# Kernel optimization log

Hardware: AMD Instinct MI355X
Metric: run time of the kernel (lower is better)

## Reference

```python
import jax, jax.numpy as jnp
import numpy as np

N = 100000   # nodes
E = 500000   # edges per relation
R = 3        # relations (etypes)
L = 2        # layers
F = 300      # input features
H = 256      # hidden
C = 23       # classes


def setup_inputs() -> dict:
    key = jax.random.key(0)
    ks = jax.random.split(key, 12)
    s = 0.05
    return {
        "x": jax.random.normal(ks[0], (N, F), jnp.float32),
        "edge_src": jax.random.randint(ks[1], (R, E), 0, N, dtype=jnp.int32),
        "edge_dst": jax.random.randint(ks[2], (R, E), 0, N, dtype=jnp.int32),
        "W_feat": jax.random.normal(ks[3], (F, H), jnp.float32) * s,
        "b_feat": jnp.zeros((H,), jnp.float32),
        "g_feat": jnp.ones((H,), jnp.float32),
        "beta_feat": jnp.zeros((H,), jnp.float32),
        "gcn_W": jax.random.normal(ks[4], (L, R, H, H), jnp.float32) * s,
        "gcn_b": jnp.zeros((L, R, H), jnp.float32),
        "skip_W": jax.random.normal(ks[5], (L, H, H), jnp.float32) * s,
        "skip_b": jnp.zeros((L, H), jnp.float32),
        "bn_g": jnp.ones((L, H), jnp.float32),
        "bn_b": jnp.zeros((L, H), jnp.float32),
        "W_c1": jax.random.normal(ks[6], (H, H), jnp.float32) * s,
        "b_c1": jnp.zeros((H,), jnp.float32),
        "g_c": jnp.ones((H,), jnp.float32),
        "beta_c": jnp.zeros((H,), jnp.float32),
        "W_c2": jax.random.normal(ks[7], (H, C), jnp.float32) * s,
        "b_c2": jnp.zeros((C,), jnp.float32),
    }


def _bn(h, g, b):
    # BatchNorm1d, training-mode batch stats (biased var), eps=1e-5
    m = h.mean(0)
    v = jnp.mean((h - m) ** 2, 0)
    return g * (h - m) * jax.lax.rsqrt(v + 1e-5) + b


def _het_forward(x, edge_src, edge_dst, W_feat, b_feat, g_feat, beta_feat,
                 gcn_W, gcn_b, skip_W, skip_b, bn_g, bn_b,
                 W_c1, b_c1, g_c, beta_c, W_c2, b_c2):
    seg = jax.ops.segment_sum
    ones = jnp.ones((E,), jnp.float32)
    # feat_reduce: Linear + BN + ReLU
    h = jax.nn.relu(_bn(x @ W_feat + b_feat, g_feat, beta_feat))  # [N, H]
    for l in range(L):
        h_res = h @ skip_W[l] + skip_b[l]
        rel = []
        for r in range(R):  # per-relation GraphConv (DGL norm='both')
            src, dst = edge_src[r], edge_dst[r]
            dout = jnp.clip(seg(ones, src, num_segments=N), 1.0, None)
            din = jnp.clip(seg(ones, dst, num_segments=N), 1.0, None)
            xs = h * jax.lax.rsqrt(dout)[:, None]          # src-normalize
            m = seg(xs[src], dst, num_segments=N)          # gather-scatter
            m = m * jax.lax.rsqrt(din)[:, None]            # dst-normalize
            rel.append(m @ gcn_W[l, r] + gcn_b[l, r])
        h = jnp.mean(jnp.stack(rel, 0), 0)  # het_combine='mean'
        h = h + h_res
        h = jax.nn.leaky_relu(_bn(h, bn_g[l], bn_b[l]), 0.01)
        # dropout is identity in eval mode
    # classification head
    h = jax.nn.relu(_bn(h @ W_c1 + b_c1, g_c, beta_c))
    return h @ W_c2 + b_c2  # [N, C]


def reference(x, edge_src, edge_dst, W_feat, b_feat, g_feat, beta_feat,
              gcn_W, gcn_b, skip_W, skip_b, bn_g, bn_b,
              W_c1, b_c1, g_c, beta_c, W_c2, b_c2):
    return _het_forward(x, edge_src, edge_dst, W_feat, b_feat, g_feat,
                        beta_feat, gcn_W, gcn_b, skip_W, skip_b, bn_g, bn_b,
                        W_c1, b_c1, g_c, beta_c, W_c2, b_c2)
```

## Files before the change

kernel.cpp:

```cpp
#include <hip/hip_runtime.h>

#define NN 100000
#define EE 500000
#define RR 3
#define LL 2
#define FF 300
#define HH 256
#define CC 23
#define MPAD 100096
#define SCHUNK 2048
#define SNB ((NN + SCHUNK - 1) / SCHUNK)

static inline int cdiv_h(int a, int b) { return (a + b - 1) / b; }

typedef __attribute__((ext_vector_type(8))) short bf16x8;
typedef __attribute__((ext_vector_type(4))) float f32x4;
typedef __attribute__((ext_vector_type(4))) unsigned short u16x4;

__device__ inline unsigned short f2bf(float f) {
    union { float f; unsigned int u; } v; v.f = f;
    unsigned int r = v.u + 0x7fff + ((v.u >> 16) & 1);
    return (unsigned short)(r >> 16);
}
__device__ inline float bf2f(unsigned short u) {
    union { unsigned int u; float f; } v; v.u = ((unsigned int)u) << 16;
    return v.f;
}
__device__ inline void gl_lds16(const void* g, void* l) {
    __builtin_amdgcn_global_load_lds((const __attribute__((address_space(1))) unsigned int*)g,
                                     (__attribute__((address_space(3))) unsigned int*)l,
                                     16, 0, 0);
}

__global__ void hist_kernel(const int* __restrict__ src, const int* __restrict__ dst,
                            int* __restrict__ cnt_out, int* __restrict__ cnt_in,
                            int RE, int Eper) {
    int i = blockIdx.x * blockDim.x + threadIdx.x;
    if (i >= RE) return;
    int r = i / Eper;
    atomicAdd(&cnt_out[r * NN + src[i]], 1);
    atomicAdd(&cnt_in[r * NN + dst[i]], 1);
}

__global__ void rs_kernel(const int* __restrict__ cnt_out, const int* __restrict__ cnt_in,
                          float* __restrict__ rs_out, float* __restrict__ rs_in, int total) {
    int i = blockIdx.x * blockDim.x + threadIdx.x;
    if (i >= total) return;
    rs_out[i] = rsqrtf(fmaxf((float)cnt_out[i], 1.0f));
    rs_in[i]  = rsqrtf(fmaxf((float)cnt_in[i], 1.0f));
}

__global__ __launch_bounds__(256) void scan_a(const int* __restrict__ cnt, int* __restrict__ bsum) {
    int r = blockIdx.y, b = blockIdx.x, t = threadIdx.x;
    const int* c = cnt + (size_t)r * NN;
    int base = b * SCHUNK;
    int s = 0;
    for (int i = t; i < SCHUNK; i += 256) {
        int idx = base + i;
        if (idx < NN) s += c[idx];
    }
#pragma unroll
    for (int o = 1; o < 64; o <<= 1) s += __shfl_xor(s, o);
    __shared__ int sh[4];
    if ((t & 63) == 0) sh[t >> 6] = s;
    __syncthreads();
    if (t == 0) bsum[r * SNB + b] = sh[0] + sh[1] + sh[2] + sh[3];
}

__global__ void scan_b(int* __restrict__ bsum, int* __restrict__ offs) {
    int r = threadIdx.x;
    if (r >= RR) return;
    int* bs = bsum + r * SNB;
    int run = 0;
    for (int i = 0; i < SNB; i++) { int v = bs[i]; bs[i] = run; run += v; }
    offs[(size_t)r * (NN + 1) + NN] = run;
}

__global__ __launch_bounds__(256) void scan_c(const int* __restrict__ cnt, const int* __restrict__ bsum,
                                              int* __restrict__ offs, int* __restrict__ cur) {
    int r = blockIdx.y, b = blockIdx.x, t = threadIdx.x;
    const int* c = cnt + (size_t)r * NN;
    int base = b * SCHUNK + t * 8;
    int v[8]; int s = 0;
#pragma unroll
    for (int j = 0; j < 8; j++) {
        int idx = base + j;
        v[j] = (idx < NN) ? c[idx] : 0;
        s += v[j];
    }
    __shared__ int sh[256];
    sh[t] = s;
    __syncthreads();
    for (int d = 1; d < 256; d <<= 1) {
        int x = (t >= d) ? sh[t - d] : 0;
        __syncthreads();
        sh[t] += x;
        __syncthreads();
    }
    int run = sh[t] - s + bsum[r * SNB + b];
    int* orow = offs + (size_t)r * (NN + 1);
    int* crow = cur + (size_t)r * NN;
#pragma unroll
    for (int j = 0; j < 8; j++) {
        int idx = base + j;
        if (idx < NN) { orow[idx] = run; crow[idx] = run; }
        run += v[j];
    }
}

__global__ void fill_kernel(const int* __restrict__ src, const int* __restrict__ dst,
                            const float* __restrict__ rs_out,
                            int* __restrict__ cur, int2* __restrict__ srcw,
                            int RE, int Eper) {
    int i = blockIdx.x * blockDim.x + threadIdx.x;
    if (i >= RE) return;
    int r = i / Eper;
    int d = dst[i];
    int s = src[i];
    float w = rs_out[r * NN + s];
    int pos = atomicAdd(&cur[r * NN + d], 1);
    srcw[(size_t)r * Eper + pos] = make_int2(s, __float_as_int(w));
}

__global__ __launch_bounds__(256) void convert_x(const float* __restrict__ x, unsigned short* __restrict__ xpad) {
    int idx = blockIdx.x * blockDim.x + threadIdx.x;
    if (idx >= MPAD * 80) return;
    int row = idx / 80, c4 = (idx - row * 80) * 4;
    ushort4 o;
    if (row < NN && c4 + 3 < FF) {
        float4 v = *(const float4*)(x + (size_t)row * FF + c4);
        o.x = f2bf(v.x); o.y = f2bf(v.y); o.z = f2bf(v.z); o.w = f2bf(v.w);
    } else {
        o.x = 0; o.y = 0; o.z = 0; o.w = 0;
    }
    *(ushort4*)(xpad + (size_t)row * 320 + c4) = o;
}

__global__ void wprep_feat(const float* __restrict__ W, unsigned short* __restrict__ Bt) {
    int n = blockIdx.x;
    int k = threadIdx.x;
    float v = (k < FF) ? W[(size_t)k * HH + n] : 0.f;
    Bt[(size_t)n * 320 + k] = f2bf(v);
}

__global__ void wprep_layer(const float* __restrict__ skipW, const float* __restrict__ gcnW,
                            unsigned short* __restrict__ Bt) {
    int idx = blockIdx.x * blockDim.x + threadIdx.x;
    int n = idx >> 10, k = idx & 1023;
    int seg = k >> 8, k2 = k & 255;
    float v = (seg == 0) ? skipW[(size_t)k2 * HH + n]
                         : gcnW[(size_t)(seg - 1) * HH * HH + (size_t)k2 * HH + n] * (1.0f / 3.0f);
    Bt[(size_t)n * 1024 + k] = f2bf(v);
}

__global__ void bias_layer(const float* __restrict__ skip_b, const float* __restrict__ gcn_b,
                           float* __restrict__ bias) {
    int t = threadIdx.x;
    bias[t] = skip_b[t] + (gcn_b[t] + gcn_b[HH + t] + gcn_b[2 * HH + t]) * (1.0f / 3.0f);
}

__global__ void wprep_c1(const float* __restrict__ W, unsigned short* __restrict__ Bt) {
    int idx = blockIdx.x * blockDim.x + threadIdx.x;
    int n = idx >> 8, k = idx & 255;
    Bt[(size_t)n * HH + k] = f2bf(W[(size_t)k * HH + n]);
}

__global__ void wprep_c2(const float* __restrict__ W, unsigned short* __restrict__ Bt) {
    int n = blockIdx.x;
    int k = threadIdx.x;
    float v = (n < CC) ? W[(size_t)k * CC + n] : 0.f;
    Bt[(size_t)n * HH + k] = f2bf(v);
}

__global__ __launch_bounds__(256) void agg_bf16(unsigned short* __restrict__ hcat,
                                                const int* __restrict__ offs_all,
                                                const int2* __restrict__ srcw_all,
                                                const float* __restrict__ rs_in_all) {
    int r = blockIdx.y;
    const int* offs = offs_all + (size_t)r * (NN + 1);
    const int2* srcw = srcw_all + (size_t)r * EE;
    const float* rs_i = rs_in_all + (size_t)r * NN;
    int wave = threadIdx.x >> 6;
    int lane = threadIdx.x & 63;
    int node = blockIdx.x * 4 + wave;
    if (node >= NN) return;
    int s0 = __builtin_amdgcn_readfirstlane(offs[node]);
    int s1 = __builtin_amdgcn_readfirstlane(offs[node + 1]);
    int cnt = s1 - s0;
    const int2* ew = srcw + s0;
    const unsigned short* hb = hcat + lane * 4;
    float a0 = 0.f, a1 = 0.f, a2 = 0.f, a3 = 0.f;
    int k = 0;
    for (; k + 8 <= cnt; k += 8) {
        int2 e[8];
#pragma unroll
        for (int q = 0; q < 8; q++) e[q] = ew[k + q];
        ushort4 hv[8];
#pragma unroll
        for (int q = 0; q < 8; q++) hv[q] = *(const ushort4*)(hb + (size_t)e[q].x * 1024);
#pragma unroll
        for (int q = 0; q < 8; q++) {
            float u = __int_as_float(e[q].y);
            a0 += u * bf2f(hv[q].x); a1 += u * bf2f(hv[q].y);
            a2 += u * bf2f(hv[q].z); a3 += u * bf2f(hv[q].w);
        }
    }
    if (k + 4 <= cnt) {
        int2 e[4];
#pragma unroll
        for (int q = 0; q < 4; q++) e[q] = ew[k + q];
        ushort4 hv[4];
#pragma unroll
        for (int q = 0; q < 4; q++) hv[q] = *(const ushort4*)(hb + (size_t)e[q].x * 1024);
#pragma unroll
        for (int q = 0; q < 4; q++) {
            float u = __int_as_float(e[q].y);
            a0 += u * bf2f(hv[q].x); a1 += u * bf2f(hv[q].y);
            a2 += u * bf2f(hv[q].z); a3 += u * bf2f(hv[q].w);
        }
        k += 4;
    }
    int rem = cnt - k;
    if (rem > 0) {
        int2 e[3];
#pragma unroll
        for (int q = 0; q < 3; q++) {
            int kk = k + q; if (kk > cnt - 1) kk = cnt - 1;
            e[q] = ew[kk];
        }
        ushort4 hv[3];
#pragma unroll
        for (int q = 0; q < 3; q++) hv[q] = *(const ushort4*)(hb + (size_t)e[q].x * 1024);
        float u0 = __int_as_float(e[0].y);
        float u1 = rem > 1 ? __int_as_float(e[1].y) : 0.f;
        float u2 = rem > 2 ? __int_as_float(e[2].y) : 0.f;
        a0 += u0 * bf2f(hv[0].x) + u1 * bf2f(hv[1].x) + u2 * bf2f(hv[2].x);
        a1 += u0 * bf2f(hv[0].y) + u1 * bf2f(hv[1].y) + u2 * bf2f(hv[2].y);
        a2 += u0 * bf2f(hv[0].z) + u1 * bf2f(hv[1].z) + u2 * bf2f(hv[2].z);
        a3 += u0 * bf2f(hv[0].w) + u1 * bf2f(hv[1].w) + u2 * bf2f(hv[2].w);
    }
    float wi = rs_i[node];
    u16x4 o;
    o.x = f2bf(a0 * wi); o.y = f2bf(a1 * wi);
    o.z = f2bf(a2 * wi); o.w = f2bf(a3 * wi);
    __builtin_nontemporal_store(o, (u16x4*)(hcat + (size_t)node * 1024 + 256 * (r + 1) + lane * 4));
}

__global__ __launch_bounds__(512, 2) void mfma_gemm(const unsigned short* __restrict__ A, int ldA,
                                                    const unsigned short* __restrict__ Bt,
                                                    const float* __restrict__ bias,
                                                    void* __restrict__ Cv, int ldC,
                                                    int Nstore, int K, int c_bf16,
                                                    float* __restrict__ stats) {
    __shared__ unsigned short lds[2][24576];
    int tid = threadIdx.x;
    int w = tid >> 6, lane = tid & 63;
    int quad = lane >> 4, lr = lane & 15;
    int bm = blockIdx.y * 128;
    int wm = w >> 2, wn = w & 3;
    int lrow = lane >> 2;
    int lslot = lane & 3;

    f32x4 acc[4][4];
#pragma unroll
    for (int i = 0; i < 4; i++)
#pragma unroll
        for (int j = 0; j < 4; j++) acc[i][j] = (f32x4){0.f, 0.f, 0.f, 0.f};

    const int NT = K >> 6;

    auto stage = [&](int bi, int t) {
        int k0 = t << 6;
        int rA = w * 16 + lrow;
        int cgA = lslot ^ ((rA >> 1) & 3);
#pragma unroll
        for (int h = 0; h < 2; h++) {
            gl_lds16(A + (size_t)(bm + rA) * ldA + k0 + h * 32 + cgA * 8,
                     &lds[bi][h * 4096 + w * 512]);
#pragma unroll
            for (int c = 0; c < 2; c++) {
                int cc = w * 2 + c;
                int rB = cc * 16 + lrow;
                int cgB = lslot ^ ((rB >> 1) & 3);
                gl_lds16(Bt + (size_t)rB * K + k0 + h * 32 + cgB * 8,
                         &lds[bi][8192 + h * 8192 + cc * 512]);
            }
        }
    };

    stage(0, 0);
    asm volatile("s_waitcnt vmcnt(0)" ::: "memory");
    __builtin_amdgcn_s_barrier();
    asm volatile("" ::: "memory");

    int cur = 0;
    for (int t = 0; t < NT; t++) {
        if (t + 1 < NT) stage(cur ^ 1, t + 1);
#pragma unroll
        for (int h = 0; h < 2; h++) {
            bf16x8 af[4], bfr[4];
#pragma unroll
            for (int i = 0; i < 4; i++) {
                int r = wm * 64 + i * 16 + lr;
                int s = quad ^ ((r >> 1) & 3);
                af[i] = *(const bf16x8*)&lds[cur][h * 4096 + r * 32 + s * 8];
            }
#pragma unroll
            for (int j = 0; j < 4; j++) {
                int n = wn * 64 + j * 16 + lr;
                int s = quad ^ ((n >> 1) & 3);
                bfr[j] = *(const bf16x8*)&lds[cur][8192 + h * 8192 + n * 32 + s * 8];
            }
#pragma unroll
            for (int i = 0; i < 4; i++)
#pragma unroll
                for (int j = 0; j < 4; j++)
                    acc[i][j] = __builtin_amdgcn_mfma_f32_16x16x32_bf16(af[i], bfr[j], acc[i][j], 0, 0, 0);
        }
        if (t + 1 < NT) {
            asm volatile("s_waitcnt vmcnt(0)" ::: "memory");
            __builtin_amdgcn_s_barrier();
            asm volatile("" ::: "memory");
        }
        cur ^= 1;
    }

    __syncthreads();

    if (c_bf16) {
        unsigned short* ldsC = &lds[0][0];
#pragma unroll
        for (int j = 0; j < 4; j++) {
            int col = wn * 64 + j * 16 + lr;
            float bv = bias ? bias[col] : 0.f;
            float ssum = 0.f, ssq = 0.f;
#pragma unroll
            for (int i = 0; i < 4; i++) {
#pragma unroll
                for (int v = 0; v < 4; v++) {
                    int row = wm * 64 + i * 16 + quad * 4 + v;
                    float val = acc[i][j][v] + bv;
                    ldsC[row * 264 + col] = f2bf(val);
                    if (bm + row < NN) { ssum += val; ssq += val * val; }
                }
            }
            if (stats) {
                ssum += __shfl_xor(ssum, 16); ssum += __shfl_xor(ssum, 32);
                ssq  += __shfl_xor(ssq, 16);  ssq  += __shfl_xor(ssq, 32);
                if (quad == 0) {
                    atomicAdd(&stats[col], ssum);
                    atomicAdd(&stats[HH + col], ssq);
                }
            }
        }
        __syncthreads();
        int row = tid >> 2, seg = tid & 3;
        if (bm + row < NN) {
            const unsigned short* srcp = ldsC + row * 264 + seg * 64;
            unsigned short* dstp = (unsigned short*)Cv + (size_t)(bm + row) * ldC + seg * 64;
#pragma unroll
            for (int q = 0; q < 8; q++)
                *(uint4*)(dstp + q * 8) = *(const uint4*)(srcp + q * 8);
        }
    } else {
        float* Cf = (float*)Cv;
#pragma unroll
        for (int j = 0; j < 4; j++) {
            int col = wn * 64 + j * 16 + lr;
            if (col >= Nstore) continue;
            float bv = bias ? bias[col] : 0.f;
#pragma unroll
            for (int i = 0; i < 4; i++) {
#pragma unroll
                for (int v = 0; v < 4; v++) {
                    int row = bm + wm * 64 + i * 16 + quad * 4 + v;
                    if (row < NN) Cf[(size_t)row * ldC + col] = acc[i][j][v] + bv;
                }
            }
        }
    }
}

__global__ void bn_coef(const float* __restrict__ stats, const float* __restrict__ g,
                        const float* __restrict__ b, float* __restrict__ coef, float invM) {
    int c = threadIdx.x;
    float mean = stats[c] * invM;
    float var = stats[HH + c] * invM - mean * mean;
    float inv = rsqrtf(var + 1e-5f);
    float sc = g[c] * inv;
    coef[c] = sc;
    coef[HH + c] = b[c] - mean * sc;
}

__global__ __launch_bounds__(256) void bn_apply_v(const unsigned short* __restrict__ Z,
                                                  const float* __restrict__ coef,
                                                  unsigned short* __restrict__ out, int act) {
    int idx = blockIdx.x * blockDim.x + threadIdx.x;
    if (idx >= NN * 32) return;
    int row = idx >> 5, cg = (idx & 31) * 8;
    union { uint4 u; unsigned short s[8]; } zin, zo;
    zin.u = *(const uint4*)(Z + (size_t)row * HH + cg);
    f32x4 sc0 = *(const f32x4*)(coef + cg);
    f32x4 sc1 = *(const f32x4*)(coef + cg + 4);
    f32x4 sh0 = *(const f32x4*)(coef + HH + cg);
    f32x4 sh1 = *(const f32x4*)(coef + HH + cg + 4);
#pragma unroll
    for (int j = 0; j < 8; j++) {
        float sc = (j < 4) ? sc0[j] : sc1[j - 4];
        float sh = (j < 4) ? sh0[j] : sh1[j - 4];
        float v = bf2f(zin.s[j]) * sc + sh;
        if (act == 1) v = fmaxf(v, 0.f);
        else v = (v < 0.f) ? 0.01f * v : v;
        zo.s[j] = f2bf(v);
    }
    *(uint4*)(out + (size_t)row * 1024 + cg) = zo.u;
}

extern "C" void kernel_launch(void* const* d_in, const int* in_sizes, int n_in,
                              void* d_out, int out_size, void* d_ws, size_t ws_size,
                              hipStream_t stream) {
    const float* x        = (const float*)d_in[0];
    const int*   esrc     = (const int*)d_in[1];
    const int*   edst     = (const int*)d_in[2];
    const float* W_feat   = (const float*)d_in[3];
    const float* b_feat   = (const float*)d_in[4];
    const float* g_feat   = (const float*)d_in[5];
    const float* beta_feat= (const float*)d_in[6];
    const float* gcn_W    = (const float*)d_in[7];
    const float* gcn_b    = (const float*)d_in[8];
    const float* skip_W   = (const float*)d_in[9];
    const float* skip_b   = (const float*)d_in[10];
    const float* bn_g     = (const float*)d_in[11];
    const float* bn_b     = (const float*)d_in[12];
    const float* W_c1     = (const float*)d_in[13];
    const float* b_c1     = (const float*)d_in[14];
    const float* g_c      = (const float*)d_in[15];
    const float* beta_c   = (const float*)d_in[16];
    const float* W_c2     = (const float*)d_in[17];
    const float* b_c2     = (const float*)d_in[18];
    float* out = (float*)d_out;
    (void)in_sizes; (void)n_in; (void)out_size; (void)ws_size;

    char* w = (char*)d_ws;
    size_t off = 0;
    auto alloc = [&](size_t bytes) { void* p = w + off; off += (bytes + 255) & ~(size_t)255; return p; };
    unsigned short* hcat = (unsigned short*)alloc((size_t)MPAD * 1024 * 2);
    unsigned short* xpad = hcat;
    unsigned short* c_acc = (unsigned short*)alloc((size_t)NN * HH * 2);
    float* f_stats = (float*)alloc(4 * 2 * HH * 4);
    float* f_coef  = (float*)alloc(2 * HH * 4);
    float* f_rs_out = (float*)alloc((size_t)RR * NN * 4);
    float* f_rs_in  = (float*)alloc((size_t)RR * NN * 4);
    int* i_cnt_out = (int*)alloc((size_t)RR * NN * 4);
    int* i_cnt_in  = (int*)alloc((size_t)RR * NN * 4);
    int* i_off     = (int*)alloc((size_t)RR * (NN + 1) * 4);
    int* i_cur     = (int*)alloc((size_t)RR * NN * 4);
    int2* i_srcw   = (int2*)alloc((size_t)RR * EE * 8);
    int* i_bsum    = (int*)alloc((size_t)RR * SNB * 4);
    unsigned short* Bt_feat = (unsigned short*)alloc(256 * 320 * 2);
    unsigned short* Bt_l0   = (unsigned short*)alloc(256 * 1024 * 2);
    unsigned short* Bt_l1   = (unsigned short*)alloc(256 * 1024 * 2);
    unsigned short* Bt_c1   = (unsigned short*)alloc(256 * 256 * 2);
    unsigned short* Bt_c2   = (unsigned short*)alloc(256 * 256 * 2);
    float* bias_l0 = (float*)alloc(HH * 4);
    float* bias_l1 = (float*)alloc(HH * 4);

    const float invM = 1.0f / (float)NN;
    const int RE = RR * EE;

    (void)hipMemsetAsync(i_cnt_out, 0, (size_t)RR * NN * 4, stream);
    (void)hipMemsetAsync(i_cnt_in, 0, (size_t)RR * NN * 4, stream);
    (void)hipMemsetAsync(f_stats, 0, 4 * 2 * HH * 4, stream);
    hist_kernel<<<cdiv_h(RE, 256), 256, 0, stream>>>(esrc, edst, i_cnt_out, i_cnt_in, RE, EE);
    rs_kernel<<<cdiv_h(RR * NN, 256), 256, 0, stream>>>(i_cnt_out, i_cnt_in, f_rs_out, f_rs_in, RR * NN);
    scan_a<<<dim3(SNB, RR), 256, 0, stream>>>(i_cnt_in, i_bsum);
    scan_b<<<1, 64, 0, stream>>>(i_bsum, i_off);
    scan_c<<<dim3(SNB, RR), 256, 0, stream>>>(i_cnt_in, i_bsum, i_off, i_cur);
    fill_kernel<<<cdiv_h(RE, 256), 256, 0, stream>>>(esrc, edst, f_rs_out, i_cur, i_srcw, RE, EE);

    convert_x<<<cdiv_h(MPAD * 80, 256), 256, 0, stream>>>(x, xpad);
    wprep_feat<<<256, 320, 0, stream>>>(W_feat, Bt_feat);
    wprep_layer<<<1024, 256, 0, stream>>>(skip_W, gcn_W, Bt_l0);
    wprep_layer<<<1024, 256, 0, stream>>>(skip_W + (size_t)HH * HH, gcn_W + (size_t)RR * HH * HH, Bt_l1);
    bias_layer<<<1, 256, 0, stream>>>(skip_b, gcn_b, bias_l0);
    bias_layer<<<1, 256, 0, stream>>>(skip_b + HH, gcn_b + (size_t)RR * HH, bias_l1);
    wprep_c1<<<256, 256, 0, stream>>>(W_c1, Bt_c1);
    wprep_c2<<<256, 256, 0, stream>>>(W_c2, Bt_c2);

    dim3 grid_G(1, MPAD / 128);
    const int nblk_a = cdiv_h(NN * 32, 256);
    float* st0 = f_stats;
    float* st1 = f_stats + 2 * HH;
    float* st2 = f_stats + 4 * HH;
    float* st3 = f_stats + 6 * HH;

    mfma_gemm<<<grid_G, 512, 0, stream>>>(xpad, 320, Bt_feat, b_feat, c_acc, HH, HH, 320, 1, st0);
    bn_coef<<<1, 256, 0, stream>>>(st0, g_feat, beta_feat, f_coef, invM);
    bn_apply_v<<<nblk_a, 256, 0, stream>>>(c_acc, f_coef, hcat, 1);

    for (int l = 0; l < LL; l++) {
        agg_bf16<<<dim3(cdiv_h(NN, 4), RR), 256, 0, stream>>>(hcat, i_off, i_srcw, f_rs_in);
        float* st = l ? st2 : st1;
        mfma_gemm<<<grid_G, 512, 0, stream>>>(hcat, 1024, l ? Bt_l1 : Bt_l0,
                                              l ? bias_l1 : bias_l0, c_acc, HH, HH, 1024, 1, st);
        bn_coef<<<1, 256, 0, stream>>>(st, bn_g + (size_t)l * HH, bn_b + (size_t)l * HH, f_coef, invM);
        bn_apply_v<<<nblk_a, 256, 0, stream>>>(c_acc, f_coef, hcat, 2);
    }

    mfma_gemm<<<grid_G, 512, 0, stream>>>(hcat, 1024, Bt_c1, b_c1, c_acc, HH, HH, 256, 1, st3);
    bn_coef<<<1, 256, 0, stream>>>(st3, g_c, beta_c, f_coef, invM);
    bn_apply_v<<<nblk_a, 256, 0, stream>>>(c_acc, f_coef, hcat + 256, 1);
    mfma_gemm<<<grid_G, 512, 0, stream>>>(hcat + 256, 1024, Bt_c2, b_c2, out, CC, CC, 256, 0, nullptr);
}
```

Baseline: 1.212 ms.

## Load GEMM B fragments directly from global memory and shrink LDS for occupancy

The B (weight) operand is no longer staged through LDS. Each wave now reads its B fragments straight from global memory into registers every K-step, and only A stays double-buffered in LDS. LDS shrinks to a single array sized for the epilogue, and launch bounds are raised to 4 blocks per CU to allow more concurrent blocks. The trade is more redundant global and L2 traffic for B across waves and blocks, plus higher register pressure under the tighter bound, possibly with spills. The B loads are also issued synchronously before the MFMA loop, so their latency may not be hidden.

```diff
diff --git a/kernel.cpp b/kernel.cpp
--- a/kernel.cpp
+++ b/kernel.cpp
@@ -246,13 +246,13 @@
     __builtin_nontemporal_store(o, (u16x4*)(hcat + (size_t)node * 1024 + 256 * (r + 1) + lane * 4));
 }
 
-__global__ __launch_bounds__(512, 2) void mfma_gemm(const unsigned short* __restrict__ A, int ldA,
+__global__ __launch_bounds__(512, 4) void mfma_gemm(const unsigned short* __restrict__ A, int ldA,
                                                     const unsigned short* __restrict__ Bt,
                                                     const float* __restrict__ bias,
                                                     void* __restrict__ Cv, int ldC,
                                                     int Nstore, int K, int c_bf16,
                                                     float* __restrict__ stats) {
-    __shared__ unsigned short lds[2][24576];
+    __shared__ unsigned short lds[33792];
     int tid = threadIdx.x;
     int w = tid >> 6, lane = tid & 63;
     int quad = lane >> 4, lr = lane & 15;
@@ -269,53 +269,48 @@
 
     const int NT = K >> 6;
 
-    auto stage = [&](int bi, int t) {
+    const unsigned short* Bbase = Bt + (size_t)(wn * 64 + lr) * K + quad * 8;
+
+    auto stageA = [&](int bi, int t) {
         int k0 = t << 6;
         int rA = w * 16 + lrow;
         int cgA = lslot ^ ((rA >> 1) & 3);
 #pragma unroll
         for (int h = 0; h < 2; h++) {
             gl_lds16(A + (size_t)(bm + rA) * ldA + k0 + h * 32 + cgA * 8,
-                     &lds[bi][h * 4096 + w * 512]);
-#pragma unroll
-            for (int c = 0; c < 2; c++) {
-                int cc = w * 2 + c;
-                int rB = cc * 16 + lrow;
-                int cgB = lslot ^ ((rB >> 1) & 3);
-                gl_lds16(Bt + (size_t)rB * K + k0 + h * 32 + cgB * 8,
-                         &lds[bi][8192 + h * 8192 + cc * 512]);
-            }
+                     &lds[bi * 8192 + h * 4096 + w * 512]);
         }
     };
 
-    stage(0, 0);
+    stageA(0, 0);
     asm volatile("s_waitcnt vmcnt(0)" ::: "memory");
     __builtin_amdgcn_s_barrier();
     asm volatile("" ::: "memory");
 
     int cur = 0;
     for (int t = 0; t < NT; t++) {
-        if (t + 1 < NT) stage(cur ^ 1, t + 1);
+        int k0 = t << 6;
+        bf16x8 bfr[2][4];
+#pragma unroll
+        for (int h = 0; h < 2; h++)
+#pragma unroll
+            for (int j = 0; j < 4; j++)
+                bfr[h][j] = *(const bf16x8*)(Bbase + (size_t)j * 16 * K + k0 + h * 32);
+        if (t + 1 < NT) stageA(cur ^ 1, t + 1);
 #pragma unroll
         for (int h = 0; h < 2; h++) {
-            bf16x8 af[4], bfr[4];
+            bf16x8 af[4];
 #pragma unroll
             for (int i = 0; i < 4; i++) {
                 int r = wm * 64 + i * 16 + lr;
                 int s = quad ^ ((r >> 1) & 3);
-                af[i] = *(const bf16x8*)&lds[cur][h * 4096 + r * 32 + s * 8];
+                af[i] = *(const bf16x8*)&lds[cur * 8192 + h * 4096 + r * 32 + s * 8];
             }
 #pragma unroll
-            for (int j = 0; j < 4; j++) {
-                int n = wn * 64 + j * 16 + lr;
-                int s = quad ^ ((n >> 1) & 3);
-                bfr[j] = *(const bf16x8*)&lds[cur][8192 + h * 8192 + n * 32 + s * 8];
-            }
-#pragma unroll
             for (int i = 0; i < 4; i++)
 #pragma unroll
                 for (int j = 0; j < 4; j++)
-                    acc[i][j] = __builtin_amdgcn_mfma_f32_16x16x32_bf16(af[i], bfr[j], acc[i][j], 0, 0, 0);
+                    acc[i][j] = __builtin_amdgcn_mfma_f32_16x16x32_bf16(af[i], bfr[h][j], acc[i][j], 0, 0, 0);
         }
         if (t + 1 < NT) {
             asm volatile("s_waitcnt vmcnt(0)" ::: "memory");
@@ -328,7 +323,7 @@
     __syncthreads();
 
     if (c_bf16) {
-        unsigned short* ldsC = &lds[0][0];
+        unsigned short* ldsC = lds;
 #pragma unroll
         for (int j = 0; j < 4; j++) {
             int col = wn * 64 + j * 16 + lr;
```

Result: slower. 1.297 ms (+7.0%).

## Split aggregation into feature halves and single-buffer GEMM for higher occupancy

Applied to the files above, without the earlier changes.

The aggregation kernel now runs twice per layer, each pass gathering only 128 of the 256 features (2 bf16 per lane instead of 4), which halves the working set each pass touches in cache. The GEMM drops its LDS double buffer for a single buffer guarded by two __syncthreads per K-step, and its launch bounds rise from 2 to 4 blocks per CU. The aim is better cache hit rates in the gather and more resident blocks in the GEMM. The costs are twice the edge-list reads and launches, narrower gather loads, and no overlap between global-to-LDS loads and MFMA compute.

```diff
diff --git a/kernel.cpp b/kernel.cpp
--- a/kernel.cpp
+++ b/kernel.cpp
@@ -15,7 +15,7 @@
 
 typedef __attribute__((ext_vector_type(8))) short bf16x8;
 typedef __attribute__((ext_vector_type(4))) float f32x4;
-typedef __attribute__((ext_vector_type(4))) unsigned short u16x4;
+typedef __attribute__((ext_vector_type(2))) unsigned short u16x2;
 
 __device__ inline unsigned short f2bf(float f) {
     union { float f; unsigned int u; } v; v.f = f;
@@ -175,7 +175,8 @@
 __global__ __launch_bounds__(256) void agg_bf16(unsigned short* __restrict__ hcat,
                                                 const int* __restrict__ offs_all,
                                                 const int2* __restrict__ srcw_all,
-                                                const float* __restrict__ rs_in_all) {
+                                                const float* __restrict__ rs_in_all,
+                                                int half) {
     int r = blockIdx.y;
     const int* offs = offs_all + (size_t)r * (NN + 1);
     const int2* srcw = srcw_all + (size_t)r * EE;
@@ -188,35 +189,33 @@
     int s1 = __builtin_amdgcn_readfirstlane(offs[node + 1]);
     int cnt = s1 - s0;
     const int2* ew = srcw + s0;
-    const unsigned short* hb = hcat + lane * 4;
-    float a0 = 0.f, a1 = 0.f, a2 = 0.f, a3 = 0.f;
+    const unsigned short* hb = hcat + half * 128 + lane * 2;
+    float a0 = 0.f, a1 = 0.f;
     int k = 0;
     for (; k + 8 <= cnt; k += 8) {
         int2 e[8];
 #pragma unroll
         for (int q = 0; q < 8; q++) e[q] = ew[k + q];
-        ushort4 hv[8];
-#pragma unroll
-        for (int q = 0; q < 8; q++) hv[q] = *(const ushort4*)(hb + (size_t)e[q].x * 1024);
+        ushort2 hv[8];
+#pragma unroll
+        for (int q = 0; q < 8; q++) hv[q] = *(const ushort2*)(hb + (size_t)e[q].x * 1024);
 #pragma unroll
         for (int q = 0; q < 8; q++) {
             float u = __int_as_float(e[q].y);
             a0 += u * bf2f(hv[q].x); a1 += u * bf2f(hv[q].y);
-            a2 += u * bf2f(hv[q].z); a3 += u * bf2f(hv[q].w);
         }
     }
     if (k + 4 <= cnt) {
         int2 e[4];
 #pragma unroll
         for (int q = 0; q < 4; q++) e[q] = ew[k + q];
-        ushort4 hv[4];
-#pragma unroll
-        for (int q = 0; q < 4; q++) hv[q] = *(const ushort4*)(hb + (size_t)e[q].x * 1024);
+        ushort2 hv[4];
+#pragma unroll
+        for (int q = 0; q < 4; q++) hv[q] = *(const ushort2*)(hb + (size_t)e[q].x * 1024);
 #pragma unroll
         for (int q = 0; q < 4; q++) {
             float u = __int_as_float(e[q].y);
             a0 += u * bf2f(hv[q].x); a1 += u * bf2f(hv[q].y);
-            a2 += u * bf2f(hv[q].z); a3 += u * bf2f(hv[q].w);
         }
         k += 4;
     }
@@ -228,31 +227,28 @@
             int kk = k + q; if (kk > cnt - 1) kk = cnt - 1;
             e[q] = ew[kk];
         }
-        ushort4 hv[3];
-#pragma unroll
-        for (int q = 0; q < 3; q++) hv[q] = *(const ushort4*)(hb + (size_t)e[q].x * 1024);
+        ushort2 hv[3];
+#pragma unroll
+        for (int q = 0; q < 3; q++) hv[q] = *(const ushort2*)(hb + (size_t)e[q].x * 1024);
         float u0 = __int_as_float(e[0].y);
         float u1 = rem > 1 ? __int_as_float(e[1].y) : 0.f;
         float u2 = rem > 2 ? __int_as_float(e[2].y) : 0.f;
         a0 += u0 * bf2f(hv[0].x) + u1 * bf2f(hv[1].x) + u2 * bf2f(hv[2].x);
         a1 += u0 * bf2f(hv[0].y) + u1 * bf2f(hv[1].y) + u2 * bf2f(hv[2].y);
-        a2 += u0 * bf2f(hv[0].z) + u1 * bf2f(hv[1].z) + u2 * bf2f(hv[2].z);
-        a3 += u0 * bf2f(hv[0].w) + u1 * bf2f(hv[1].w) + u2 * bf2f(hv[2].w);
     }
     float wi = rs_i[node];
-    u16x4 o;
+    u16x2 o;
     o.x = f2bf(a0 * wi); o.y = f2bf(a1 * wi);
-    o.z = f2bf(a2 * wi); o.w = f2bf(a3 * wi);
-    __builtin_nontemporal_store(o, (u16x4*)(hcat + (size_t)node * 1024 + 256 * (r + 1) + lane * 4));
-}
-
-__global__ __launch_bounds__(512, 2) void mfma_gemm(const unsigned short* __restrict__ A, int ldA,
+    __builtin_nontemporal_store(o, (u16x2*)(hcat + (size_t)node * 1024 + 256 * (r + 1) + half * 128 + lane * 2));
+}
+
+__global__ __launch_bounds__(512, 4) void mfma_gemm(const unsigned short* __restrict__ A, int ldA,
                                                     const unsigned short* __restrict__ Bt,
                                                     const float* __restrict__ bias,
                                                     void* __restrict__ Cv, int ldC,
                                                     int Nstore, int K, int c_bf16,
                                                     float* __restrict__ stats) {
-    __shared__ unsigned short lds[2][24576];
+    __shared__ unsigned short lds[33792];
     int tid = threadIdx.x;
     int w = tid >> 6, lane = tid & 63;
     int quad = lane >> 4, lr = lane & 15;
@@ -267,35 +263,23 @@
 #pragma unroll
         for (int j = 0; j < 4; j++) acc[i][j] = (f32x4){0.f, 0.f, 0.f, 0.f};
 
-    const int NT = K >> 6;
-
-    auto stage = [&](int bi, int t) {
-        int k0 = t << 6;
+    for (int k0 = 0; k0 < K; k0 += 64) {
         int rA = w * 16 + lrow;
         int cgA = lslot ^ ((rA >> 1) & 3);
 #pragma unroll
         for (int h = 0; h < 2; h++) {
             gl_lds16(A + (size_t)(bm + rA) * ldA + k0 + h * 32 + cgA * 8,
-                     &lds[bi][h * 4096 + w * 512]);
+                     &lds[h * 4096 + w * 512]);
 #pragma unroll
             for (int c = 0; c < 2; c++) {
                 int cc = w * 2 + c;
                 int rB = cc * 16 + lrow;
                 int cgB = lslot ^ ((rB >> 1) & 3);
                 gl_lds16(Bt + (size_t)rB * K + k0 + h * 32 + cgB * 8,
-                         &lds[bi][8192 + h * 8192 + cc * 512]);
-            }
-        }
-    };
-
-    stage(0, 0);
-    asm volatile("s_waitcnt vmcnt(0)" ::: "memory");
-    __builtin_amdgcn_s_barrier();
-    asm volatile("" ::: "memory");
-
-    int cur = 0;
-    for (int t = 0; t < NT; t++) {
-        if (t + 1 < NT) stage(cur ^ 1, t + 1);
+                         &lds[8192 + h * 8192 + cc * 512]);
+            }
+        }
+        __syncthreads();
 #pragma unroll
         for (int h = 0; h < 2; h++) {
             bf16x8 af[4], bfr[4];
@@ -303,13 +287,13 @@
             for (int i = 0; i < 4; i++) {
                 int r = wm * 64 + i * 16 + lr;
                 int s = quad ^ ((r >> 1) & 3);
-                af[i] = *(const bf16x8*)&lds[cur][h * 4096 + r * 32 + s * 8];
+                af[i] = *(const bf16x8*)&lds[h * 4096 + r * 32 + s * 8];
             }
 #pragma unroll
             for (int j = 0; j < 4; j++) {
                 int n = wn * 64 + j * 16 + lr;
                 int s = quad ^ ((n >> 1) & 3);
-                bfr[j] = *(const bf16x8*)&lds[cur][8192 + h * 8192 + n * 32 + s * 8];
+                bfr[j] = *(const bf16x8*)&lds[8192 + h * 8192 + n * 32 + s * 8];
             }
 #pragma unroll
             for (int i = 0; i < 4; i++)
@@ -317,18 +301,11 @@
                 for (int j = 0; j < 4; j++)
                     acc[i][j] = __builtin_amdgcn_mfma_f32_16x16x32_bf16(af[i], bfr[j], acc[i][j], 0, 0, 0);
         }
-        if (t + 1 < NT) {
-            asm volatile("s_waitcnt vmcnt(0)" ::: "memory");
-            __builtin_amdgcn_s_barrier();
-            asm volatile("" ::: "memory");
-        }
-        cur ^= 1;
-    }
-
-    __syncthreads();
+        __syncthreads();
+    }
 
     if (c_bf16) {
-        unsigned short* ldsC = &lds[0][0];
+        unsigned short* ldsC = lds;
 #pragma unroll
         for (int j = 0; j < 4; j++) {
             int col = wn * 64 + j * 16 + lr;
@@ -488,6 +465,7 @@
     wprep_c2<<<256, 256, 0, stream>>>(W_c2, Bt_c2);
 
     dim3 grid_G(1, MPAD / 128);
+    dim3 grid_A(cdiv_h(NN, 4), RR);
     const int nblk_a = cdiv_h(NN * 32, 256);
     float* st0 = f_stats;
     float* st1 = f_stats + 2 * HH;
@@ -499,7 +477,8 @@
     bn_apply_v<<<nblk_a, 256, 0, stream>>>(c_acc, f_coef, hcat, 1);
 
     for (int l = 0; l < LL; l++) {
-        agg_bf16<<<dim3(cdiv_h(NN, 4), RR), 256, 0, stream>>>(hcat, i_off, i_srcw, f_rs_in);
+        agg_bf16<<<grid_A, 256, 0, stream>>>(hcat, i_off, i_srcw, f_rs_in, 0);
+        agg_bf16<<<grid_A, 256, 0, stream>>>(hcat, i_off, i_srcw, f_rs_in, 1);
         float* st = l ? st2 : st1;
         mfma_gemm<<<grid_G, 512, 0, stream>>>(hcat, 1024, l ? Bt_l1 : Bt_l0,
                                               l ? bias_l1 : bias_l0, c_acc, HH, HH, 1024, 1, st);
```

Measured after the change: 1.232 ms. No clear change (+1.7%).
